# Kernel tuning notes

Hardware: AMD Instinct MI355X
Metric: run time of the kernel (lower is better)

## Reference

```python
import jax, jax.numpy as jnp
import numpy as np

DIM, HEADS, DIM_HEAD = 1024, 16, 64


def setup_inputs() -> dict:
    key = jax.random.key(0)
    k1, k2, k3, k4 = jax.random.split(key, 4)
    x = jax.random.normal(k1, (4, 2048, DIM), dtype=jnp.float32)
    # nn.Linear(dim, 3*dim, bias=False): weight [3*dim, dim]; y = x @ W.T
    W_qkv = jax.random.normal(k2, (3 * DIM, DIM), dtype=jnp.float32) * (DIM ** -0.5)
    W_proj = jax.random.normal(k3, (DIM, DIM), dtype=jnp.float32) * (DIM ** -0.5)
    b_proj = jax.random.normal(k4, (DIM,), dtype=jnp.float32) * 0.02
    return {"x": x, "W_qkv": W_qkv, "W_proj": W_proj, "b_proj": b_proj}


def reference(x, W_qkv, W_proj, b_proj):
    B, N, C = x.shape
    H, D = HEADS, DIM_HEAD
    scale = D ** -0.5
    qkv = x @ W_qkv.T                                   # [B, N, 3C]
    qkv = qkv.reshape(B, N, 3, H, D).transpose(2, 0, 3, 1, 4)  # [3, B, H, N, D]
    q, k, v = qkv[0], qkv[1], qkv[2]
    dots = jnp.einsum('bhid,bhjd->bhij', q, k) * scale  # [B, H, N, N]
    attn = jax.nn.softmax(dots, axis=-1)
    out = jnp.einsum('bhij,bhjd->bhid', attn, v)        # [B, H, N, D]
    out = out.transpose(0, 2, 1, 3).reshape(B, N, C)
    return out @ W_proj.T + b_proj
```

## Files before the change

### kernel.cpp

```cpp
#include <hip/hip_runtime.h>
#include <hip/hip_bf16.h>
#include <stdint.h>

typedef __bf16 bf16x4 __attribute__((ext_vector_type(4)));
typedef __bf16 bf16x8 __attribute__((ext_vector_type(8)));
typedef float  f32x4  __attribute__((ext_vector_type(4)));

#define LOG2E 1.44269504088896f

__device__ __forceinline__ void gl2lds16(const __bf16* g, __bf16* l) {
    __builtin_amdgcn_global_load_lds(
        (const __attribute__((address_space(1))) void*)g,
        (__attribute__((address_space(3))) void*)l, 16, 0, 0);
}

__global__ __launch_bounds__(256) void cvt3_f32_bf16(
    const float* __restrict__ x,  __bf16* __restrict__ xb,
    const float* __restrict__ wq, __bf16* __restrict__ wqb,
    const float* __restrict__ wp, __bf16* __restrict__ wpb) {
    const int bid = blockIdx.x;
    const float* in; __bf16* out; int base;
    if (bid < 4096)      { in = x;  out = xb;  base = bid; }
    else if (bid < 5632) { in = wq; out = wqb; base = bid - 4096; }
    else                 { in = wp; out = wpb; base = bid - 5632; }
    size_t i = ((size_t)base * 256 + threadIdx.x) * 8;
    float4 a = ((const float4*)(in + i))[0];
    float4 b = ((const float4*)(in + i))[1];
    bf16x8 v;
    v[0] = (__bf16)a.x; v[1] = (__bf16)a.y; v[2] = (__bf16)a.z; v[3] = (__bf16)a.w;
    v[4] = (__bf16)b.x; v[5] = (__bf16)b.y; v[6] = (__bf16)b.z; v[7] = (__bf16)b.w;
    *(bf16x8*)(out + i) = v;
}

template<typename TC>
__global__ __launch_bounds__(512, 2) void gemm_8ph(
    const __bf16* __restrict__ A, const __bf16* __restrict__ B,
    const float* __restrict__ bias, TC* __restrict__ C,
    int M, int N, int K, int lda, int ldb, int ldc)
{
    __shared__ __bf16 As[2][256][64];
    __shared__ __bf16 Bs[2][256][64];

    const int tid = threadIdx.x;
    const int wave = tid >> 6, l = tid & 63;
    const int lr = l & 15, lq = l >> 4;
    const int wm = wave >> 2, wn = wave & 3;
    const int m0 = blockIdx.y * 256, n0 = blockIdx.x * 256;

    const int cswz = (lq * 8) ^ ((lr & 1) << 5);
    const int cswz1 = cswz ^ 32;

    const int srow = l >> 3;
    const int selem = ((l & 7) * 8) ^ (((l >> 3) & 1) << 5);

    const int rA[4] = { wm*128 + wn*16, wm*128 + wn*16 + 8,
                        wm*128 + 64 + wn*16, wm*128 + 64 + wn*16 + 8 };
    const int hb = wn >> 1, q = wm * 2 + (wn & 1);
    const int rB[4] = { hb*128 + q*32, hb*128 + q*32 + 8,
                        hb*128 + q*32 + 16, hb*128 + q*32 + 24 };

    const __bf16* gA[4]; const __bf16* gB[4];
#pragma unroll
    for (int s = 0; s < 4; ++s) {
        gA[s] = A + (size_t)(m0 + rA[s] + srow) * lda + selem;
        gB[s] = B + (size_t)(n0 + rB[s] + srow) * ldb + selem;
    }

    const int T = K >> 6;
    f32x4 acc[8][4] = {};

#define STA(buf, s, kt) gl2lds16(gA[s] + ((kt) << 6), &As[buf][rA[s]][0])
#define STB(buf, s, kt) gl2lds16(gB[s] + ((kt) << 6), &Bs[buf][rB[s]][0])

    STA(0, 0, 0); STA(0, 1, 0); STA(0, 2, 0); STA(0, 3, 0);
    STB(0, 0, 0); STB(0, 1, 0); STB(0, 2, 0); STB(0, 3, 0);
    if (T > 1) {
        STA(1, 0, 1); STA(1, 1, 1);
        asm volatile("s_waitcnt vmcnt(2)" ::: "memory");
    } else {
        asm volatile("s_waitcnt vmcnt(0)" ::: "memory");
    }
    __builtin_amdgcn_s_barrier();

    bf16x8 bf[4];
    for (int t = 0; t < T; ++t) {
        const int cur = t & 1, nxt = cur ^ 1;

        {
            bf16x8 af[4];
#pragma unroll
            for (int i = 0; i < 4; ++i)
                af[i] = *(const bf16x8*)&As[cur][wm*128 + i*16 + lr][cswz];
#pragma unroll
            for (int j = 0; j < 4; ++j)
                bf[j] = *(const bf16x8*)&Bs[cur][wn*64 + j*16 + lr][cswz];
            if (t + 1 < T) { STA(nxt, 2, t + 1); STA(nxt, 3, t + 1); }
            __builtin_amdgcn_s_barrier();
            asm volatile("s_waitcnt lgkmcnt(0)" ::: "memory");
            __builtin_amdgcn_s_setprio(1);
#pragma unroll
            for (int i = 0; i < 4; ++i)
#pragma unroll
                for (int j = 0; j < 4; ++j)
                    acc[i][j] = __builtin_amdgcn_mfma_f32_16x16x32_bf16(bf[j], af[i], acc[i][j], 0, 0, 0);
            __builtin_amdgcn_s_setprio(0);
            __builtin_amdgcn_s_barrier();
        }
        {
            bf16x8 af[4];
#pragma unroll
            for (int i = 0; i < 4; ++i)
                af[i] = *(const bf16x8*)&As[cur][wm*128 + 64 + i*16 + lr][cswz];
            if (t + 1 < T) { STB(nxt, 0, t + 1); STB(nxt, 1, t + 1); }
            __builtin_amdgcn_s_barrier();
            asm volatile("s_waitcnt lgkmcnt(0)" ::: "memory");
            __builtin_amdgcn_s_setprio(1);
#pragma unroll
            for (int i = 0; i < 4; ++i)
#pragma unroll
                for (int j = 0; j < 4; ++j)
                    acc[4 + i][j] = __builtin_amdgcn_mfma_f32_16x16x32_bf16(bf[j], af[i], acc[4 + i][j], 0, 0, 0);
            __builtin_amdgcn_s_setprio(0);
            __builtin_amdgcn_s_barrier();
        }
        {
            bf16x8 af[4];
#pragma unroll
            for (int i = 0; i < 4; ++i)
                af[i] = *(const bf16x8*)&As[cur][wm*128 + i*16 + lr][cswz1];
#pragma unroll
            for (int j = 0; j < 4; ++j)
                bf[j] = *(const bf16x8*)&Bs[cur][wn*64 + j*16 + lr][cswz1];
            if (t + 1 < T) { STB(nxt, 2, t + 1); STB(nxt, 3, t + 1); }
            __builtin_amdgcn_s_barrier();
            asm volatile("s_waitcnt lgkmcnt(0)" ::: "memory");
            __builtin_amdgcn_s_setprio(1);
#pragma unroll
            for (int i = 0; i < 4; ++i)
#pragma unroll
                for (int j = 0; j < 4; ++j)
                    acc[i][j] = __builtin_amdgcn_mfma_f32_16x16x32_bf16(bf[j], af[i], acc[i][j], 0, 0, 0);
            __builtin_amdgcn_s_setprio(0);
            __builtin_amdgcn_s_barrier();
        }
        {
            bf16x8 af[4];
#pragma unroll
            for (int i = 0; i < 4; ++i)
                af[i] = *(const bf16x8*)&As[cur][wm*128 + 64 + i*16 + lr][cswz1];
            if (t + 2 < T) { STA(cur, 0, t + 2); STA(cur, 1, t + 2); }
            __builtin_amdgcn_s_barrier();
            asm volatile("s_waitcnt lgkmcnt(0)" ::: "memory");
            __builtin_amdgcn_s_setprio(1);
#pragma unroll
            for (int i = 0; i < 4; ++i)
#pragma unroll
                for (int j = 0; j < 4; ++j)
                    acc[4 + i][j] = __builtin_amdgcn_mfma_f32_16x16x32_bf16(bf[j], af[i], acc[4 + i][j], 0, 0, 0);
            __builtin_amdgcn_s_setprio(0);
            if (t + 2 < T) {
                asm volatile("s_waitcnt vmcnt(2)" ::: "memory");
                __builtin_amdgcn_s_barrier();
            } else if (t + 1 < T) {
                asm volatile("s_waitcnt vmcnt(0)" ::: "memory");
                __builtin_amdgcn_s_barrier();
            }
        }
    }
#undef STA
#undef STB

    float4 bv4[4] = {{0.f,0.f,0.f,0.f},{0.f,0.f,0.f,0.f},{0.f,0.f,0.f,0.f},{0.f,0.f,0.f,0.f}};
    if (bias)
#pragma unroll
        for (int j = 0; j < 4; ++j)
            bv4[j] = *(const float4*)&bias[n0 + wn*64 + j*16 + lq*4];
#pragma unroll
    for (int ii = 0; ii < 8; ++ii) {
        const int row = m0 + wm*128 + ii*16 + lr;
#pragma unroll
        for (int j = 0; j < 4; ++j) {
            const int col = n0 + wn*64 + j*16 + lq*4;
            if constexpr (sizeof(TC) == 2) {
                bf16x4 ob;
                ob[0] = (__bf16)(acc[ii][j][0] + bv4[j].x);
                ob[1] = (__bf16)(acc[ii][j][1] + bv4[j].y);
                ob[2] = (__bf16)(acc[ii][j][2] + bv4[j].z);
                ob[3] = (__bf16)(acc[ii][j][3] + bv4[j].w);
                *(bf16x4*)&C[(size_t)row * ldc + col] = ob;
            } else {
                float4 ov;
                ov.x = acc[ii][j][0] + bv4[j].x;
                ov.y = acc[ii][j][1] + bv4[j].y;
                ov.z = acc[ii][j][2] + bv4[j].z;
                ov.w = acc[ii][j][3] + bv4[j].w;
                *(float4*)&C[(size_t)row * ldc + col] = ov;
            }
        }
    }
}

__device__ __forceinline__ void stage16(const float* __restrict__ g, __bf16* l) {
    float4 a = ((const float4*)g)[0];
    float4 b = ((const float4*)g)[1];
    float4 c = ((const float4*)g)[2];
    float4 d = ((const float4*)g)[3];
    bf16x8 lo, hi;
    lo[0] = (__bf16)a.x; lo[1] = (__bf16)a.y; lo[2] = (__bf16)a.z; lo[3] = (__bf16)a.w;
    lo[4] = (__bf16)b.x; lo[5] = (__bf16)b.y; lo[6] = (__bf16)b.z; lo[7] = (__bf16)b.w;
    hi[0] = (__bf16)c.x; hi[1] = (__bf16)c.y; hi[2] = (__bf16)c.z; hi[3] = (__bf16)c.w;
    hi[4] = (__bf16)d.x; hi[5] = (__bf16)d.y; hi[6] = (__bf16)d.z; hi[7] = (__bf16)d.w;
    ((bf16x8*)l)[0] = lo;
    ((bf16x8*)l)[1] = hi;
}
__device__ __forceinline__ void stage16(const __bf16* __restrict__ g, __bf16* l) {
    ((bf16x8*)l)[0] = ((const bf16x8*)g)[0];
    ((bf16x8*)l)[1] = ((const bf16x8*)g)[1];
}

template<typename TA, typename TB, typename TC>
__global__ __launch_bounds__(256) void gemm_bt(
    const TA* __restrict__ A, const TB* __restrict__ B,
    const float* __restrict__ bias, TC* __restrict__ C,
    int M, int N, int K, int lda, int ldb, int ldc)
{
    __shared__ __bf16 As[128][40];
    __shared__ __bf16 Bs[128][40];
    const int tid = threadIdx.x;
    const int wave = tid >> 6, lane = tid & 63;
    const int lr = lane & 15, lq = lane >> 4;
    const int m0 = blockIdx.y * 128, n0 = blockIdx.x * 128;
    const int wm = (wave >> 1) * 64, wn = (wave & 1) * 64;
    const int srow = tid >> 1, scol = (tid & 1) * 16;

    f32x4 acc[4][4] = {};
    const TA* agp = A + (size_t)(m0 + srow) * lda + scol;
    const TB* bgp = B + (size_t)(n0 + srow) * ldb + scol;

    for (int k0 = 0; k0 < K; k0 += 32) {
        __syncthreads();
        stage16(agp + k0, &As[srow][scol]);
        stage16(bgp + k0, &Bs[srow][scol]);
        __syncthreads();
        bf16x8 af[4], bf[4];
        for (int i = 0; i < 4; ++i) af[i] = *(const bf16x8*)&As[wm + i * 16 + lr][lq * 8];
        for (int j = 0; j < 4; ++j) bf[j] = *(const bf16x8*)&Bs[wn + j * 16 + lr][lq * 8];
        for (int i = 0; i < 4; ++i)
            for (int j = 0; j < 4; ++j)
                acc[i][j] = __builtin_amdgcn_mfma_f32_16x16x32_bf16(bf[j], af[i], acc[i][j], 0, 0, 0);
    }

    float4 bv4[4] = {{0.f,0.f,0.f,0.f},{0.f,0.f,0.f,0.f},{0.f,0.f,0.f,0.f},{0.f,0.f,0.f,0.f}};
    if (bias)
        for (int j = 0; j < 4; ++j)
            bv4[j] = *(const float4*)&bias[n0 + wn + j * 16 + lq * 4];
    for (int i = 0; i < 4; ++i) {
        const int row = m0 + wm + i * 16 + lr;
        for (int j = 0; j < 4; ++j) {
            const int col = n0 + wn + j * 16 + lq * 4;
            if constexpr (sizeof(TC) == 2) {
                bf16x4 ob;
                ob[0] = (__bf16)(acc[i][j][0] + bv4[j].x);
                ob[1] = (__bf16)(acc[i][j][1] + bv4[j].y);
                ob[2] = (__bf16)(acc[i][j][2] + bv4[j].z);
                ob[3] = (__bf16)(acc[i][j][3] + bv4[j].w);
                *(bf16x4*)&C[(size_t)row * ldc + col] = ob;
            } else {
                float4 ov;
                ov.x = acc[i][j][0] + bv4[j].x;
                ov.y = acc[i][j][1] + bv4[j].y;
                ov.z = acc[i][j][2] + bv4[j].z;
                ov.w = acc[i][j][3] + bv4[j].w;
                *(float4*)&C[(size_t)row * ldc + col] = ov;
            }
        }
    }
}

__global__ __launch_bounds__(512, 4) void attn_kernel(__bf16* __restrict__ qkv)
{
    __shared__ __bf16 Ks[2][64][72];
    __shared__ __bf16 Vt[2][64][72];

    const int tid = threadIdx.x;
    const int wave = tid >> 6, lane = tid & 63;
    const int lr = lane & 15, lq = lane >> 4;

    const int bid = blockIdx.x;
    const int xcd = bid & 7, slot = bid >> 3;
    const int bh = xcd * 8 + (slot >> 3);
    const int qt = slot & 7;
    const int b = bh >> 4, h = bh & 15;
    const int rowbase = b * 2048;
    const int q0 = qt * 256;
    const float c1 = 0.125f * LOG2E;

    bf16x8 qf[2][2];
    for (int mt = 0; mt < 2; ++mt)
        for (int ks = 0; ks < 2; ++ks) {
            bf16x8 v = *(const bf16x8*)(qkv +
                (size_t)(rowbase + q0 + wave * 32 + mt * 16 + lr) * 3072 + h * 64 + ks * 32 + lq * 8);
            bf16x8 w;
            for (int e = 0; e < 8; ++e) w[e] = (__bf16)((float)v[e] * c1);
            qf[mt][ks] = w;
        }

    bf16x8 ones8;
    for (int e = 0; e < 8; ++e) ones8[e] = (__bf16)1.0f;

    f32x4 l_acc[2] = {};
    f32x4 o_acc[2][4] = {};

    const int tid2 = tid & 255;
    const int kr = tid2 >> 2, kc = (tid2 & 3) * 16;
    const int g0 = tid2 & 15;
    const int vj0 = g0 * 4, vd0 = (tid2 >> 4) * 4;
    const int vcol = ((g0 >> 3) * 32) + ((g0 & 3) * 8) + (((g0 >> 2) & 1) * 4);
    const __bf16* kbase = qkv + (size_t)(rowbase + kr) * 3072 + 1024 + h * 64 + kc;
    const __bf16* vbase = qkv + (size_t)(rowbase + vj0) * 3072 + 2048 + h * 64 + vd0;

    bf16x8 ka, kb;
    uint2 t0, t1, t2, t3;

    if (wave >= 4) {
        ka = ((const bf16x8*)kbase)[0];
        kb = ((const bf16x8*)kbase)[1];
        *(bf16x8*)&Ks[0][kr][kc] = ka;
        *(bf16x8*)(&Ks[0][kr][kc] + 8) = kb;
    } else {
        t0 = *(const uint2*)(vbase);
        t1 = *(const uint2*)(vbase + 3072);
        t2 = *(const uint2*)(vbase + 6144);
        t3 = *(const uint2*)(vbase + 9216);
        uint2 c0 = { (t0.x & 0xffffu) | (t1.x << 16), (t2.x & 0xffffu) | (t3.x << 16) };
        uint2 d1 = { (t0.x >> 16) | (t1.x & 0xffff0000u), (t2.x >> 16) | (t3.x & 0xffff0000u) };
        uint2 c2 = { (t0.y & 0xffffu) | (t1.y << 16), (t2.y & 0xffffu) | (t3.y << 16) };
        uint2 d3 = { (t0.y >> 16) | (t1.y & 0xffff0000u), (t2.y >> 16) | (t3.y & 0xffff0000u) };
        *(uint2*)&Vt[0][vd0 + 0][vcol] = c0;
        *(uint2*)&Vt[0][vd0 + 1][vcol] = d1;
        *(uint2*)&Vt[0][vd0 + 2][vcol] = c2;
        *(uint2*)&Vt[0][vd0 + 3][vcol] = d3;
    }

    for (int it = 0; it < 32; ++it) {
        const int cur = it & 1;
        __syncthreads();

        if (it + 1 < 32) {
            if (wave >= 4) {
                const __bf16* kg = kbase + (size_t)(it + 1) * 64 * 3072;
                ka = ((const bf16x8*)kg)[0];
                kb = ((const bf16x8*)kg)[1];
            } else {
                const __bf16* vg = vbase + (size_t)(it + 1) * 64 * 3072;
                t0 = *(const uint2*)(vg);
                t1 = *(const uint2*)(vg + 3072);
                t2 = *(const uint2*)(vg + 6144);
                t3 = *(const uint2*)(vg + 9216);
            }
        }

        for (int pi = 0; pi < 2; ++pi) {
            f32x4 s[2][2] = {};
            for (int ks = 0; ks < 2; ++ks) {
                bf16x8 kf0 = *(const bf16x8*)&Ks[cur][(2 * pi + 0) * 16 + lr][ks * 32 + lq * 8];
                bf16x8 kf1 = *(const bf16x8*)&Ks[cur][(2 * pi + 1) * 16 + lr][ks * 32 + lq * 8];
                for (int mt = 0; mt < 2; ++mt) {
                    s[mt][0] = __builtin_amdgcn_mfma_f32_16x16x32_bf16(kf0, qf[mt][ks], s[mt][0], 0, 0, 0);
                    s[mt][1] = __builtin_amdgcn_mfma_f32_16x16x32_bf16(kf1, qf[mt][ks], s[mt][1], 0, 0, 0);
                }
            }
            bf16x8 pfrag[2];
            for (int mt = 0; mt < 2; ++mt) {
                for (int t = 0; t < 2; ++t)
                    for (int r = 0; r < 4; ++r) {
                        float p = __builtin_amdgcn_exp2f(s[mt][t][r]);
                        pfrag[mt][t * 4 + r] = (__bf16)p;
                    }
            }
            for (int mt = 0; mt < 2; ++mt)
                l_acc[mt] = __builtin_amdgcn_mfma_f32_16x16x32_bf16(ones8, pfrag[mt], l_acc[mt], 0, 0, 0);
            for (int dt = 0; dt < 4; ++dt) {
                bf16x8 vf = *(const bf16x8*)&Vt[cur][dt * 16 + lr][pi * 32 + lq * 8];
                for (int mt = 0; mt < 2; ++mt)
                    o_acc[mt][dt] = __builtin_amdgcn_mfma_f32_16x16x32_bf16(vf, pfrag[mt], o_acc[mt][dt], 0, 0, 0);
            }
        }

        if (it + 1 < 32) {
            const int nb = cur ^ 1;
            if (wave >= 4) {
                *(bf16x8*)&Ks[nb][kr][kc] = ka;
                *(bf16x8*)(&Ks[nb][kr][kc] + 8) = kb;
            } else {
                uint2 c0 = { (t0.x & 0xffffu) | (t1.x << 16), (t2.x & 0xffffu) | (t3.x << 16) };
                uint2 d1 = { (t0.x >> 16) | (t1.x & 0xffff0000u), (t2.x >> 16) | (t3.x & 0xffff0000u) };
                uint2 c2 = { (t0.y & 0xffffu) | (t1.y << 16), (t2.y & 0xffffu) | (t3.y << 16) };
                uint2 d3 = { (t0.y >> 16) | (t1.y & 0xffff0000u), (t2.y >> 16) | (t3.y & 0xffff0000u) };
                *(uint2*)&Vt[nb][vd0 + 0][vcol] = c0;
                *(uint2*)&Vt[nb][vd0 + 1][vcol] = d1;
                *(uint2*)&Vt[nb][vd0 + 2][vcol] = c2;
                *(uint2*)&Vt[nb][vd0 + 3][vcol] = d3;
            }
        }
    }

    for (int mt = 0; mt < 2; ++mt) {
        float inv = 1.f / l_acc[mt][0];
        for (int dt = 0; dt < 4; ++dt) {
            bf16x4 ob;
            for (int r = 0; r < 4; ++r) ob[r] = (__bf16)(o_acc[mt][dt][r] * inv);
            *(bf16x4*)(qkv + (size_t)(rowbase + q0 + wave * 32 + mt * 16 + lr) * 3072 +
                       h * 64 + dt * 16 + lq * 4) = ob;
        }
    }
}

extern "C" void kernel_launch(void* const* d_in, const int* in_sizes, int n_in,
                              void* d_out, int out_size, void* d_ws, size_t ws_size,
                              hipStream_t stream) {
    const float* x     = (const float*)d_in[0];
    const float* Wqkv  = (const float*)d_in[1];
    const float* Wproj = (const float*)d_in[2];
    const float* bproj = (const float*)d_in[3];
    float* out   = (float*)d_out;
    __bf16* qkvb = (__bf16*)d_ws;

    const size_t QKV_E = (size_t)8192 * 3072;
    const size_t X_E   = (size_t)8192 * 1024;
    const size_t WQ_E  = (size_t)3072 * 1024;
    const size_t WP_E  = (size_t)1024 * 1024;
    const bool fast = ws_size >= (QKV_E + X_E + WQ_E + WP_E) * sizeof(__bf16);

    if (fast) {
        __bf16* xb  = qkvb + QKV_E;
        __bf16* wqb = xb + X_E;
        __bf16* wpb = wqb + WQ_E;
        cvt3_f32_bf16<<<dim3(6144), 256, 0, stream>>>(x, xb, Wqkv, wqb, Wproj, wpb);
        gemm_8ph<__bf16><<<dim3(12, 32), 512, 0, stream>>>(
            xb, wqb, nullptr, qkvb, 8192, 3072, 1024, 1024, 1024, 3072);
        attn_kernel<<<dim3(512), 512, 0, stream>>>(qkvb);
        gemm_8ph<float><<<dim3(4, 32), 512, 0, stream>>>(
            qkvb, wpb, bproj, out, 8192, 1024, 1024, 3072, 1024, 1024);
    } else {
        gemm_bt<float, float, __bf16><<<dim3(24, 64), 256, 0, stream>>>(
            x, Wqkv, nullptr, qkvb, 8192, 3072, 1024, 1024, 1024, 3072);
        attn_kernel<<<dim3(512), 512, 0, stream>>>(qkvb);
        gemm_bt<__bf16, float, float><<<dim3(8, 64), 256, 0, stream>>>(
            qkvb, Wproj, bproj, out, 8192, 1024, 1024, 3072, 1024, 1024);
    }
}
```

Baseline: 298.4 us.

## Widen LDS swizzle in 8-phase GEMM and use smaller-tile GEMM for projection

The LDS XOR swizzle in gemm_8ph changes from a 2-row pattern to an 8-row pattern, on both the global-to-LDS write side and the fragment read side. The goal is fewer LDS bank conflicts in the QKV GEMM. The output projection moves from the 256x256 gemm_8ph (only 128 blocks) to a new 128x128 bf16 kernel launched as 512 blocks, which loads tiles directly into LDS with global_load_lds. This should fill the GPU better for the small projection GEMM, but the new kernel is single-buffered and its LDS layout is unpadded, so fragment reads may hit bank conflicts.

```diff
diff --git a/kernel.cpp b/kernel.cpp
--- a/kernel.cpp
+++ b/kernel.cpp
@@ -47,11 +47,11 @@
     const int wm = wave >> 2, wn = wave & 3;
     const int m0 = blockIdx.y * 256, n0 = blockIdx.x * 256;
 
-    const int cswz = (lq * 8) ^ ((lr & 1) << 5);
+    const int cswz  = (lq * 8) ^ ((lr & 7) << 3);
     const int cswz1 = cswz ^ 32;
 
-    const int srow = l >> 3;
-    const int selem = ((l & 7) * 8) ^ (((l >> 3) & 1) << 5);
+    const int srow  = l >> 3;
+    const int selem = (((l & 7) ^ (l >> 3)) << 3);
 
     const int rA[4] = { wm*128 + wn*16, wm*128 + wn*16 + 8,
                         wm*128 + 64 + wn*16, wm*128 + 64 + wn*16 + 8 };
@@ -200,47 +200,40 @@
     }
 }
 
-__device__ __forceinline__ void stage16(const float* __restrict__ g, __bf16* l) {
-    float4 a = ((const float4*)g)[0];
-    float4 b = ((const float4*)g)[1];
-    float4 c = ((const float4*)g)[2];
-    float4 d = ((const float4*)g)[3];
-    bf16x8 lo, hi;
-    lo[0] = (__bf16)a.x; lo[1] = (__bf16)a.y; lo[2] = (__bf16)a.z; lo[3] = (__bf16)a.w;
-    lo[4] = (__bf16)b.x; lo[5] = (__bf16)b.y; lo[6] = (__bf16)b.z; lo[7] = (__bf16)b.w;
-    hi[0] = (__bf16)c.x; hi[1] = (__bf16)c.y; hi[2] = (__bf16)c.z; hi[3] = (__bf16)c.w;
-    hi[4] = (__bf16)d.x; hi[5] = (__bf16)d.y; hi[6] = (__bf16)d.z; hi[7] = (__bf16)d.w;
-    ((bf16x8*)l)[0] = lo;
-    ((bf16x8*)l)[1] = hi;
-}
-__device__ __forceinline__ void stage16(const __bf16* __restrict__ g, __bf16* l) {
-    ((bf16x8*)l)[0] = ((const bf16x8*)g)[0];
-    ((bf16x8*)l)[1] = ((const bf16x8*)g)[1];
-}
-
-template<typename TA, typename TB, typename TC>
-__global__ __launch_bounds__(256) void gemm_bt(
-    const TA* __restrict__ A, const TB* __restrict__ B,
+template<typename TC>
+__global__ __launch_bounds__(256) void gemm_bt_bf16(
+    const __bf16* __restrict__ A, const __bf16* __restrict__ B,
     const float* __restrict__ bias, TC* __restrict__ C,
     int M, int N, int K, int lda, int ldb, int ldc)
 {
-    __shared__ __bf16 As[128][40];
-    __shared__ __bf16 Bs[128][40];
+    __shared__ __bf16 As[128][32];
+    __shared__ __bf16 Bs[128][32];
     const int tid = threadIdx.x;
     const int wave = tid >> 6, lane = tid & 63;
     const int lr = lane & 15, lq = lane >> 4;
     const int m0 = blockIdx.y * 128, n0 = blockIdx.x * 128;
     const int wm = (wave >> 1) * 64, wn = (wave & 1) * 64;
-    const int srow = tid >> 1, scol = (tid & 1) * 16;
 
     f32x4 acc[4][4] = {};
-    const TA* agp = A + (size_t)(m0 + srow) * lda + scol;
-    const TB* bgp = B + (size_t)(n0 + srow) * ldb + scol;
+
+    const int sr = lane >> 2;
+    const int sc = (lane & 3) * 8;
+    const __bf16* ag[2]; const __bf16* bg[2];
+    __bf16* alds[2]; __bf16* blds[2];
+    for (int t = 0; t < 2; ++t) {
+        int chunk = wave * 2 + t;
+        ag[t] = A + (size_t)(m0 + chunk * 16 + sr) * lda + sc;
+        bg[t] = B + (size_t)(n0 + chunk * 16 + sr) * ldb + sc;
+        alds[t] = &As[0][0] + chunk * 512;
+        blds[t] = &Bs[0][0] + chunk * 512;
+    }
 
     for (int k0 = 0; k0 < K; k0 += 32) {
         __syncthreads();
-        stage16(agp + k0, &As[srow][scol]);
-        stage16(bgp + k0, &Bs[srow][scol]);
+        gl2lds16(ag[0] + k0, alds[0]);
+        gl2lds16(ag[1] + k0, alds[1]);
+        gl2lds16(bg[0] + k0, blds[0]);
+        gl2lds16(bg[1] + k0, blds[1]);
         __syncthreads();
         bf16x8 af[4], bf[4];
         for (int i = 0; i < 4; ++i) af[i] = *(const bf16x8*)&As[wm + i * 16 + lr][lq * 8];
@@ -277,6 +270,83 @@
     }
 }
 
+__device__ __forceinline__ void stage16(const float* __restrict__ g, __bf16* l) {
+    float4 a = ((const float4*)g)[0];
+    float4 b = ((const float4*)g)[1];
+    float4 c = ((const float4*)g)[2];
+    float4 d = ((const float4*)g)[3];
+    bf16x8 lo, hi;
+    lo[0] = (__bf16)a.x; lo[1] = (__bf16)a.y; lo[2] = (__bf16)a.z; lo[3] = (__bf16)a.w;
+    lo[4] = (__bf16)b.x; lo[5] = (__bf16)b.y; lo[6] = (__bf16)b.z; lo[7] = (__bf16)b.w;
+    hi[0] = (__bf16)c.x; hi[1] = (__bf16)c.y; hi[2] = (__bf16)c.z; hi[3] = (__bf16)c.w;
+    hi[4] = (__bf16)d.x; hi[5] = (__bf16)d.y; hi[6] = (__bf16)d.z; hi[7] = (__bf16)d.w;
+    ((bf16x8*)l)[0] = lo;
+    ((bf16x8*)l)[1] = hi;
+}
+__device__ __forceinline__ void stage16(const __bf16* __restrict__ g, __bf16* l) {
+    ((bf16x8*)l)[0] = ((const bf16x8*)g)[0];
+    ((bf16x8*)l)[1] = ((const bf16x8*)g)[1];
+}
+
+template<typename TA, typename TB, typename TC>
+__global__ __launch_bounds__(256) void gemm_bt(
+    const TA* __restrict__ A, const TB* __restrict__ B,
+    const float* __restrict__ bias, TC* __restrict__ C,
+    int M, int N, int K, int lda, int ldb, int ldc)
+{
+    __shared__ __bf16 As[128][40];
+    __shared__ __bf16 Bs[128][40];
+    const int tid = threadIdx.x;
+    const int wave = tid >> 6, lane = tid & 63;
+    const int lr = lane & 15, lq = lane >> 4;
+    const int m0 = blockIdx.y * 128, n0 = blockIdx.x * 128;
+    const int wm = (wave >> 1) * 64, wn = (wave & 1) * 64;
+    const int srow = tid >> 1, scol = (tid & 1) * 16;
+
+    f32x4 acc[4][4] = {};
+    const TA* agp = A + (size_t)(m0 + srow) * lda + scol;
+    const TB* bgp = B + (size_t)(n0 + srow) * ldb + scol;
+
+    for (int k0 = 0; k0 < K; k0 += 32) {
+        __syncthreads();
+        stage16(agp + k0, &As[srow][scol]);
+        stage16(bgp + k0, &Bs[srow][scol]);
+        __syncthreads();
+        bf16x8 af[4], bf[4];
+        for (int i = 0; i < 4; ++i) af[i] = *(const bf16x8*)&As[wm + i * 16 + lr][lq * 8];
+        for (int j = 0; j < 4; ++j) bf[j] = *(const bf16x8*)&Bs[wn + j * 16 + lr][lq * 8];
+        for (int i = 0; i < 4; ++i)
+            for (int j = 0; j < 4; ++j)
+                acc[i][j] = __builtin_amdgcn_mfma_f32_16x16x32_bf16(bf[j], af[i], acc[i][j], 0, 0, 0);
+    }
+
+    float4 bv4[4] = {{0.f,0.f,0.f,0.f},{0.f,0.f,0.f,0.f},{0.f,0.f,0.f,0.f},{0.f,0.f,0.f,0.f}};
+    if (bias)
+        for (int j = 0; j < 4; ++j)
+            bv4[j] = *(const float4*)&bias[n0 + wn + j * 16 + lq * 4];
+    for (int i = 0; i < 4; ++i) {
+        const int row = m0 + wm + i * 16 + lr;
+        for (int j = 0; j < 4; ++j) {
+            const int col = n0 + wn + j * 16 + lq * 4;
+            if constexpr (sizeof(TC) == 2) {
+                bf16x4 ob;
+                ob[0] = (__bf16)(acc[i][j][0] + bv4[j].x);
+                ob[1] = (__bf16)(acc[i][j][1] + bv4[j].y);
+                ob[2] = (__bf16)(acc[i][j][2] + bv4[j].z);
+                ob[3] = (__bf16)(acc[i][j][3] + bv4[j].w);
+                *(bf16x4*)&C[(size_t)row * ldc + col] = ob;
+            } else {
+                float4 ov;
+                ov.x = acc[i][j][0] + bv4[j].x;
+                ov.y = acc[i][j][1] + bv4[j].y;
+                ov.z = acc[i][j][2] + bv4[j].z;
+                ov.w = acc[i][j][3] + bv4[j].w;
+                *(float4*)&C[(size_t)row * ldc + col] = ov;
+            }
+        }
+    }
+}
+
 __global__ __launch_bounds__(512, 4) void attn_kernel(__bf16* __restrict__ qkv)
 {
     __shared__ __bf16 Ks[2][64][72];
@@ -440,7 +510,7 @@
         gemm_8ph<__bf16><<<dim3(12, 32), 512, 0, stream>>>(
             xb, wqb, nullptr, qkvb, 8192, 3072, 1024, 1024, 1024, 3072);
         attn_kernel<<<dim3(512), 512, 0, stream>>>(qkvb);
-        gemm_8ph<float><<<dim3(4, 32), 512, 0, stream>>>(
+        gemm_bt_bf16<float><<<dim3(8, 64), 256, 0, stream>>>(
             qkvb, wpb, bproj, out, 8192, 1024, 1024, 3072, 1024, 1024);
     } else {
         gemm_bt<float, float, __bf16><<<dim3(24, 64), 256, 0, stream>>>(
```

Result: faster. 269.4 us (-9.7%).

## Shrink GEMM M-tile to 128 rows and widen LDS swizzle

Applied to the files above, without the earlier changes.

Changes the bf16 GEMM block tile from 256x256 to 128x256. This doubles the grid for both the QKV and output projections, so more workgroups fill the CUs (384/128 blocks before vs 768/256 after). The A-tile loads are split between two wave groups at different phases. The LDS swizzle now XORs with three row bits instead of one to cut bank conflicts. In exchange, arithmetic intensity per block falls and B-tile global traffic rises.

```diff
diff --git a/kernel.cpp b/kernel.cpp
--- a/kernel.cpp
+++ b/kernel.cpp
@@ -33,49 +33,50 @@
 }
 
 template<typename TC>
-__global__ __launch_bounds__(512, 2) void gemm_8ph(
+__global__ __launch_bounds__(512, 2) void gemm_8ph2(
     const __bf16* __restrict__ A, const __bf16* __restrict__ B,
     const float* __restrict__ bias, TC* __restrict__ C,
     int M, int N, int K, int lda, int ldb, int ldc)
 {
-    __shared__ __bf16 As[2][256][64];
+    __shared__ __bf16 As[2][128][64];
     __shared__ __bf16 Bs[2][256][64];
 
     const int tid = threadIdx.x;
     const int wave = tid >> 6, l = tid & 63;
     const int lr = l & 15, lq = l >> 4;
     const int wm = wave >> 2, wn = wave & 3;
-    const int m0 = blockIdx.y * 256, n0 = blockIdx.x * 256;
-
-    const int cswz = (lq * 8) ^ ((lr & 1) << 5);
+    const int m0 = blockIdx.y * 128, n0 = blockIdx.x * 256;
+
+    const int cswz  = (lq * 8) ^ ((lr & 7) << 3);
     const int cswz1 = cswz ^ 32;
 
-    const int srow = l >> 3;
-    const int selem = ((l & 7) * 8) ^ (((l >> 3) & 1) << 5);
-
-    const int rA[4] = { wm*128 + wn*16, wm*128 + wn*16 + 8,
-                        wm*128 + 64 + wn*16, wm*128 + 64 + wn*16 + 8 };
-    const int hb = wn >> 1, q = wm * 2 + (wn & 1);
-    const int rB[4] = { hb*128 + q*32, hb*128 + q*32 + 8,
-                        hb*128 + q*32 + 16, hb*128 + q*32 + 24 };
-
-    const __bf16* gA[4]; const __bf16* gB[4];
-#pragma unroll
-    for (int s = 0; s < 4; ++s) {
-        gA[s] = A + (size_t)(m0 + rA[s] + srow) * lda + selem;
-        gB[s] = B + (size_t)(n0 + rB[s] + srow) * ldb + selem;
-    }
+    const int srow  = l >> 3;
+    const int selem = (((l & 7) ^ (l >> 3)) << 3);
+
+    const int g1 = (wave >> 1) & 1;
+    const int abase = (wave >> 2) * 64 + g1 * 32 + (wave & 1) * 16;
+    const int rA0 = abase, rA1 = abase + 8;
+    const int rB0 = wave * 32;
+
+    const __bf16* gA0 = A + (size_t)(m0 + rA0 + srow) * lda + selem;
+    const __bf16* gA1 = A + (size_t)(m0 + rA1 + srow) * lda + selem;
+    const __bf16* gB0 = B + (size_t)(n0 + rB0 +  0 + srow) * ldb + selem;
+    const __bf16* gB1 = B + (size_t)(n0 + rB0 +  8 + srow) * ldb + selem;
+    const __bf16* gB2 = B + (size_t)(n0 + rB0 + 16 + srow) * ldb + selem;
+    const __bf16* gB3 = B + (size_t)(n0 + rB0 + 24 + srow) * ldb + selem;
 
     const int T = K >> 6;
-    f32x4 acc[8][4] = {};
-
-#define STA(buf, s, kt) gl2lds16(gA[s] + ((kt) << 6), &As[buf][rA[s]][0])
-#define STB(buf, s, kt) gl2lds16(gB[s] + ((kt) << 6), &Bs[buf][rB[s]][0])
-
-    STA(0, 0, 0); STA(0, 1, 0); STA(0, 2, 0); STA(0, 3, 0);
-    STB(0, 0, 0); STB(0, 1, 0); STB(0, 2, 0); STB(0, 3, 0);
-    if (T > 1) {
-        STA(1, 0, 1); STA(1, 1, 1);
+    f32x4 acc[4][4] = {};
+
+    gl2lds16(gA0, &As[0][rA0][0]);
+    gl2lds16(gA1, &As[0][rA1][0]);
+    gl2lds16(gB0, &Bs[0][rB0 +  0][0]);
+    gl2lds16(gB1, &Bs[0][rB0 +  8][0]);
+    gl2lds16(gB2, &Bs[0][rB0 + 16][0]);
+    gl2lds16(gB3, &Bs[0][rB0 + 24][0]);
+    if (T > 1 && !g1) {
+        gl2lds16(gA0 + 64, &As[1][rA0][0]);
+        gl2lds16(gA1 + 64, &As[1][rA1][0]);
         asm volatile("s_waitcnt vmcnt(2)" ::: "memory");
     } else {
         asm volatile("s_waitcnt vmcnt(0)" ::: "memory");
@@ -85,21 +86,25 @@
     bf16x8 bf[4];
     for (int t = 0; t < T; ++t) {
         const int cur = t & 1, nxt = cur ^ 1;
+        const int ko  = (t + 1) << 6;
 
         {
-            bf16x8 af[4];
-#pragma unroll
-            for (int i = 0; i < 4; ++i)
-                af[i] = *(const bf16x8*)&As[cur][wm*128 + i*16 + lr][cswz];
+            bf16x8 af[2];
+#pragma unroll
+            for (int i = 0; i < 2; ++i)
+                af[i] = *(const bf16x8*)&As[cur][wm*64 + i*16 + lr][cswz];
 #pragma unroll
             for (int j = 0; j < 4; ++j)
                 bf[j] = *(const bf16x8*)&Bs[cur][wn*64 + j*16 + lr][cswz];
-            if (t + 1 < T) { STA(nxt, 2, t + 1); STA(nxt, 3, t + 1); }
+            if (t + 1 < T) {
+                gl2lds16(gB0 + ko, &Bs[nxt][rB0 + 0][0]);
+                gl2lds16(gB1 + ko, &Bs[nxt][rB0 + 8][0]);
+            }
             __builtin_amdgcn_s_barrier();
             asm volatile("s_waitcnt lgkmcnt(0)" ::: "memory");
             __builtin_amdgcn_s_setprio(1);
 #pragma unroll
-            for (int i = 0; i < 4; ++i)
+            for (int i = 0; i < 2; ++i)
 #pragma unroll
                 for (int j = 0; j < 4; ++j)
                     acc[i][j] = __builtin_amdgcn_mfma_f32_16x16x32_bf16(bf[j], af[i], acc[i][j], 0, 0, 0);
@@ -107,36 +112,42 @@
             __builtin_amdgcn_s_barrier();
         }
         {
-            bf16x8 af[4];
-#pragma unroll
-            for (int i = 0; i < 4; ++i)
-                af[i] = *(const bf16x8*)&As[cur][wm*128 + 64 + i*16 + lr][cswz];
-            if (t + 1 < T) { STB(nxt, 0, t + 1); STB(nxt, 1, t + 1); }
+            bf16x8 af[2];
+#pragma unroll
+            for (int i = 0; i < 2; ++i)
+                af[i] = *(const bf16x8*)&As[cur][wm*64 + (2 + i)*16 + lr][cswz];
+            if (t + 1 < T) {
+                gl2lds16(gB2 + ko, &Bs[nxt][rB0 + 16][0]);
+                gl2lds16(gB3 + ko, &Bs[nxt][rB0 + 24][0]);
+            }
             __builtin_amdgcn_s_barrier();
             asm volatile("s_waitcnt lgkmcnt(0)" ::: "memory");
             __builtin_amdgcn_s_setprio(1);
 #pragma unroll
-            for (int i = 0; i < 4; ++i)
+            for (int i = 0; i < 2; ++i)
 #pragma unroll
                 for (int j = 0; j < 4; ++j)
-                    acc[4 + i][j] = __builtin_amdgcn_mfma_f32_16x16x32_bf16(bf[j], af[i], acc[4 + i][j], 0, 0, 0);
+                    acc[2 + i][j] = __builtin_amdgcn_mfma_f32_16x16x32_bf16(bf[j], af[i], acc[2 + i][j], 0, 0, 0);
             __builtin_amdgcn_s_setprio(0);
             __builtin_amdgcn_s_barrier();
         }
         {
-            bf16x8 af[4];
-#pragma unroll
-            for (int i = 0; i < 4; ++i)
-                af[i] = *(const bf16x8*)&As[cur][wm*128 + i*16 + lr][cswz1];
+            bf16x8 af[2];
+#pragma unroll
+            for (int i = 0; i < 2; ++i)
+                af[i] = *(const bf16x8*)&As[cur][wm*64 + i*16 + lr][cswz1];
 #pragma unroll
             for (int j = 0; j < 4; ++j)
                 bf[j] = *(const bf16x8*)&Bs[cur][wn*64 + j*16 + lr][cswz1];
-            if (t + 1 < T) { STB(nxt, 2, t + 1); STB(nxt, 3, t + 1); }
+            if (t + 1 < T && g1) {
+                gl2lds16(gA0 + ko, &As[nxt][rA0][0]);
+                gl2lds16(gA1 + ko, &As[nxt][rA1][0]);
+            }
             __builtin_amdgcn_s_barrier();
             asm volatile("s_waitcnt lgkmcnt(0)" ::: "memory");
             __builtin_amdgcn_s_setprio(1);
 #pragma unroll
-            for (int i = 0; i < 4; ++i)
+            for (int i = 0; i < 2; ++i)
 #pragma unroll
                 for (int j = 0; j < 4; ++j)
                     acc[i][j] = __builtin_amdgcn_mfma_f32_16x16x32_bf16(bf[j], af[i], acc[i][j], 0, 0, 0);
@@ -144,22 +155,26 @@
             __builtin_amdgcn_s_barrier();
         }
         {
-            bf16x8 af[4];
-#pragma unroll
-            for (int i = 0; i < 4; ++i)
-                af[i] = *(const bf16x8*)&As[cur][wm*128 + 64 + i*16 + lr][cswz1];
-            if (t + 2 < T) { STA(cur, 0, t + 2); STA(cur, 1, t + 2); }
+            bf16x8 af[2];
+#pragma unroll
+            for (int i = 0; i < 2; ++i)
+                af[i] = *(const bf16x8*)&As[cur][wm*64 + (2 + i)*16 + lr][cswz1];
+            if (t + 2 < T && !g1) {
+                gl2lds16(gA0 + ko + 64, &As[cur][rA0][0]);
+                gl2lds16(gA1 + ko + 64, &As[cur][rA1][0]);
+            }
             __builtin_amdgcn_s_barrier();
             asm volatile("s_waitcnt lgkmcnt(0)" ::: "memory");
             __builtin_amdgcn_s_setprio(1);
 #pragma unroll
-            for (int i = 0; i < 4; ++i)
+            for (int i = 0; i < 2; ++i)
 #pragma unroll
                 for (int j = 0; j < 4; ++j)
-                    acc[4 + i][j] = __builtin_amdgcn_mfma_f32_16x16x32_bf16(bf[j], af[i], acc[4 + i][j], 0, 0, 0);
+                    acc[2 + i][j] = __builtin_amdgcn_mfma_f32_16x16x32_bf16(bf[j], af[i], acc[2 + i][j], 0, 0, 0);
             __builtin_amdgcn_s_setprio(0);
             if (t + 2 < T) {
-                asm volatile("s_waitcnt vmcnt(2)" ::: "memory");
+                if (!g1) asm volatile("s_waitcnt vmcnt(2)" ::: "memory");
+                else     asm volatile("s_waitcnt vmcnt(0)" ::: "memory");
                 __builtin_amdgcn_s_barrier();
             } else if (t + 1 < T) {
                 asm volatile("s_waitcnt vmcnt(0)" ::: "memory");
@@ -167,8 +182,6 @@
             }
         }
     }
-#undef STA
-#undef STB
 
     float4 bv4[4] = {{0.f,0.f,0.f,0.f},{0.f,0.f,0.f,0.f},{0.f,0.f,0.f,0.f},{0.f,0.f,0.f,0.f}};
     if (bias)
@@ -176,8 +189,8 @@
         for (int j = 0; j < 4; ++j)
             bv4[j] = *(const float4*)&bias[n0 + wn*64 + j*16 + lq*4];
 #pragma unroll
-    for (int ii = 0; ii < 8; ++ii) {
-        const int row = m0 + wm*128 + ii*16 + lr;
+    for (int ii = 0; ii < 4; ++ii) {
+        const int row = m0 + wm*64 + ii*16 + lr;
 #pragma unroll
         for (int j = 0; j < 4; ++j) {
             const int col = n0 + wn*64 + j*16 + lq*4;
@@ -437,10 +450,10 @@
         __bf16* wqb = xb + X_E;
         __bf16* wpb = wqb + WQ_E;
         cvt3_f32_bf16<<<dim3(6144), 256, 0, stream>>>(x, xb, Wqkv, wqb, Wproj, wpb);
-        gemm_8ph<__bf16><<<dim3(12, 32), 512, 0, stream>>>(
+        gemm_8ph2<__bf16><<<dim3(12, 64), 512, 0, stream>>>(
             xb, wqb, nullptr, qkvb, 8192, 3072, 1024, 1024, 1024, 3072);
         attn_kernel<<<dim3(512), 512, 0, stream>>>(qkvb);
-        gemm_8ph<float><<<dim3(4, 32), 512, 0, stream>>>(
+        gemm_8ph2<float><<<dim3(4, 64), 512, 0, stream>>>(
             qkvb, wpb, bproj, out, 8192, 1024, 1024, 3072, 1024, 1024);
     } else {
         gemm_bt<float, float, __bf16><<<dim3(24, 64), 256, 0, stream>>>(
```

New measurement: 278.2 us. 6.8% less time.
